# Optimization experiments

Measured on AMD Instinct MI355X. Metric: run time of the kernel, lower is better.

The kernel has to match this reference:

```python
import jax, jax.numpy as jnp
import numpy as np
from jax import lax

HEADS = 8
DIM_HEAD = 64
DIM = HEADS * DIM_HEAD  # 512


def _dwconv(x_nchw, w):
    # depthwise 3x3, stride 1, pad 1 (SAME), groups = channels
    return lax.conv_general_dilated(
        x_nchw, w, window_strides=(1, 1), padding='SAME',
        feature_group_count=x_nchw.shape[1],
        dimension_numbers=('NCHW', 'OIHW', 'NCHW'))


def setup_inputs() -> dict:
    key = jax.random.key(0)
    ks = jax.random.split(key, 9)
    b, h, w, c = 4, 256, 256, DIM
    s = 1.0 / np.sqrt(c)
    return {
        'x_in':    jax.random.normal(ks[0], (b, h, w, c), jnp.float32),
        'Wq':      jax.random.normal(ks[1], (c, DIM), jnp.float32) * s,
        'Wk':      jax.random.normal(ks[2], (c, DIM), jnp.float32) * s,
        'Wv':      jax.random.normal(ks[3], (c, DIM), jnp.float32) * s,
        'rescale': jnp.ones((HEADS, 1, 1), jnp.float32),
        'proj_w':  jax.random.normal(ks[4], (DIM, c), jnp.float32) * s,
        'proj_b':  jnp.zeros((c,), jnp.float32),
        'conv1_w': jax.random.normal(ks[5], (c, 1, 3, 3), jnp.float32) * (1.0 / 3.0),
        'conv2_w': jax.random.normal(ks[6], (c, 1, 3, 3), jnp.float32) * (1.0 / 3.0),
    }


def reference(x_in, Wq, Wk, Wv, rescale, proj_w, proj_b, conv1_w, conv2_w):
    b, h, w, c = x_in.shape
    n = h * w
    x = x_in.reshape(b, n, c)
    q_inp = x @ Wq  # [b, n, heads*d]
    k_inp = x @ Wk
    v_inp = x @ Wv

    def heads_dn(t):  # [b, n, heads*d] -> [b, heads, d, n]
        return t.reshape(b, n, HEADS, DIM_HEAD).transpose(0, 2, 3, 1)

    q = heads_dn(q_inp)
    k = heads_dn(k_inp)
    v = heads_dn(v_inp)

    # L2-normalize along token axis (F.normalize, eps=1e-12)
    qn = q / jnp.maximum(jnp.linalg.norm(q, axis=-1, keepdims=True), 1e-12)
    kn = k / jnp.maximum(jnp.linalg.norm(k, axis=-1, keepdims=True), 1e-12)

    # channel attention: [b, heads, d, d]
    attn = jnp.einsum('bhdn,bhen->bhde', kn, qn) * rescale
    attn = jax.nn.softmax(attn, axis=-1)
    xo = jnp.einsum('bhde,bhen->bhdn', attn, v)  # [b, heads, d, n]

    xo = xo.transpose(0, 3, 1, 2).reshape(b, n, HEADS * DIM_HEAD)
    out_c = (xo @ proj_w + proj_b).reshape(b, h, w, c)

    # depthwise conv positional embedding on v_inp
    vp = v_inp.reshape(b, h, w, c).transpose(0, 3, 1, 2)  # NCHW
    vp = _dwconv(vp, conv1_w)
    vp = jax.nn.gelu(vp, approximate=False)
    vp = _dwconv(vp, conv2_w)
    out_p = vp.transpose(0, 2, 3, 1)

    return out_c + out_p
```

## Files before the change

### kernel.cpp

```cpp
#include <hip/hip_runtime.h>
#include <math.h>

typedef unsigned short u16;
typedef unsigned int   u32;
typedef __attribute__((ext_vector_type(4))) float f32x4;
typedef __attribute__((ext_vector_type(8))) short bf16x8;
typedef __attribute__((ext_vector_type(8))) u16   u16x8;
typedef __attribute__((ext_vector_type(4))) u16   u16x4;

#define DEVI static __device__ __forceinline__

DEVI float bf2f(u16 a){ u32 u=((u32)a)<<16; float f; __builtin_memcpy(&f,&u,4); return f; }
DEVI u16 f2bf(float f){ u32 u; __builtin_memcpy(&u,&f,4); u=u+0x7fffu+((u>>16)&1u); return (u16)(u>>16); }

DEVI void gload16(const u16* src, u16* lds){
  __builtin_amdgcn_global_load_lds((const __attribute__((address_space(1))) u32*)src,
                                   (__attribute__((address_space(3))) u32*)lds, 16, 0, 0);
}

__global__ void k_wvt(const float* __restrict__ Wv, u16* __restrict__ WvT){
  int n = blockIdx.x;
  for (int k = threadIdx.x; k < 512; k += 256)
    WvT[(size_t)n*512 + k] = f2bf(Wv[(size_t)k*512 + n]);
}
__global__ void k_wrep(const float* __restrict__ w1, const float* __restrict__ w2, float* __restrict__ wt){
  int s = blockIdx.x/9, tap = blockIdx.x%9, c = threadIdx.x;
  const float* w = s ? w2 : w1;
  wt[(size_t)(s*9+tap)*512 + c] = w[(size_t)c*9 + tap];
}

__global__ __launch_bounds__(1024, 4) void k_gemm_v(const float* __restrict__ x, const u16* __restrict__ WvT,
                                                    u16* __restrict__ v, u16* __restrict__ xbT){
  __shared__ __align__(16) u16 Al[128*64];
  __shared__ __align__(16) u16 Bl[512*64];
  const int tid = threadIdx.x;
  const int l = tid & 63, w = tid >> 6;
  const int wr = w >> 3, wc = w & 7;
  const long r0 = (long)blockIdx.x * 128;
  f32x4 acc[4][4] = {};
  const int arow = tid >> 3, ac = tid & 7;
  const float* xp = x + (r0 + arow)*512 + ac*8;
  f32x4 va = *(const f32x4*)xp, vb = *(const f32x4*)(xp+4);
  for (int k0 = 0; k0 < 512; k0 += 64){
    {
      u16x8 o;
      o[0]=f2bf(va.x); o[1]=f2bf(va.y); o[2]=f2bf(va.z); o[3]=f2bf(va.w);
      o[4]=f2bf(vb.x); o[5]=f2bf(vb.y); o[6]=f2bf(vb.z); o[7]=f2bf(vb.w);
      *(u16x8*)&Al[arow*64 + ((ac ^ (arow&7))*8)] = o;
    }
    if (k0 < 448){
      va = *(const f32x4*)(xp + k0 + 64);
      vb = *(const f32x4*)(xp + k0 + 68);
    }
    #pragma unroll
    for (int i = 0; i < 4; ++i){
      int blkrow = w*32 + i*8;
      int r = blkrow + (l>>3);
      const u16* src = WvT + (size_t)r*512 + k0 + (((l&7) ^ ((l>>3)&7))*8);
      gload16(src, &Bl[blkrow*64]);
    }
    __syncthreads();
    #pragma unroll
    for (int ks = 0; ks < 2; ++ks){
      bf16x8 af[4], bfr[4];
      #pragma unroll
      for (int mf = 0; mf < 4; ++mf){
        int row = wr*64 + mf*16 + (l&15);
        af[mf] = *(const bf16x8*)&Al[row*64 + (((ks*4 + (l>>4)) ^ (row&7))*8)];
      }
      #pragma unroll
      for (int nf = 0; nf < 4; ++nf){
        int row = wc*64 + nf*16 + (l&15);
        bfr[nf] = *(const bf16x8*)&Bl[row*64 + (((ks*4 + (l>>4)) ^ (row&7))*8)];
      }
      #pragma unroll
      for (int mf = 0; mf < 4; ++mf)
        #pragma unroll
        for (int nf = 0; nf < 4; ++nf)
          acc[mf][nf] = __builtin_amdgcn_mfma_f32_16x16x32_bf16(af[mf], bfr[nf], acc[mf][nf], 0,0,0);
    }
    {
      int chloc = tid & 63, tg = tid >> 6;
      u16x8 o;
      #pragma unroll
      for (int j = 0; j < 8; ++j){
        int tok = tg*8 + j;
        o[j] = Al[tok*64 + (((chloc>>3) ^ (tok&7))*8) + (chloc&7)];
      }
      *(u16x8*)(xbT + (size_t)(k0 + chloc)*262144 + r0 + tg*8) = o;
    }
    __syncthreads();
  }
  #pragma unroll
  for (int mf = 0; mf < 4; ++mf)
    #pragma unroll
    for (int nf = 0; nf < 4; ++nf){
      int col = wc*64 + nf*16 + (l&15);
      #pragma unroll
      for (int j = 0; j < 4; ++j){
        long row = r0 + wr*64 + mf*16 + (l>>4)*4 + j;
        v[(size_t)row*512 + col] = f2bf(acc[mf][nf][j]);
      }
    }
}

__global__ __launch_bounds__(1024, 4) void k_syrk(const u16* __restrict__ xbT, float* __restrict__ P){
  __shared__ __align__(16) u16 AL[256*64];
  __shared__ __align__(16) u16 BL[256*64];
  const int bid = blockIdx.x;
  const int cs = bid & 63, combo = (bid>>6)%3, b = bid/192;
  const int hA = (combo==2) ? 1 : 0;
  const int tid = threadIdx.x;
  const int l = tid & 63, w = tid>>6, wi = w>>2, wj = w&3;
  const long tokb0 = (long)b*65536 + (long)cs*1024;
  const u16* Bread = (combo==1) ? BL : AL;
  f32x4 acc[4][4] = {};
  for (int st = 0; st < 16; ++st){
    const long tokb = tokb0 + st*64;
    #pragma unroll
    for (int i = 0; i < 2; ++i){
      int blkrow = w*16 + i*8;
      int r = blkrow + (l>>3);
      const u16* src = xbT + (size_t)(hA*256 + r)*262144 + tokb + (((l&7) ^ ((l>>3)&7))*8);
      gload16(src, &AL[blkrow*64]);
    }
    if (combo == 1){
      #pragma unroll
      for (int i = 0; i < 2; ++i){
        int blkrow = w*16 + i*8;
        int r = blkrow + (l>>3);
        const u16* src = xbT + (size_t)(256 + r)*262144 + tokb + (((l&7) ^ ((l>>3)&7))*8);
        gload16(src, &BL[blkrow*64]);
      }
    }
    __syncthreads();
    #pragma unroll
    for (int ks = 0; ks < 2; ++ks){
      bf16x8 af[4], bfr[4];
      #pragma unroll
      for (int mf = 0; mf < 4; ++mf){
        int row = wi*64 + mf*16 + (l&15);
        af[mf] = *(const bf16x8*)&AL[row*64 + (((ks*4 + (l>>4)) ^ (row&7))*8)];
      }
      #pragma unroll
      for (int nf = 0; nf < 4; ++nf){
        int row = wj*64 + nf*16 + (l&15);
        bfr[nf] = *(const bf16x8*)&Bread[row*64 + (((ks*4 + (l>>4)) ^ (row&7))*8)];
      }
      #pragma unroll
      for (int mf = 0; mf < 4; ++mf)
        #pragma unroll
        for (int nf = 0; nf < 4; ++nf)
          acc[mf][nf] = __builtin_amdgcn_mfma_f32_16x16x32_bf16(af[mf], bfr[nf], acc[mf][nf], 0,0,0);
    }
    __syncthreads();
  }
  float* Pb = P + (size_t)bid*65536;
  #pragma unroll
  for (int mf = 0; mf < 4; ++mf)
    #pragma unroll
    for (int nf = 0; nf < 4; ++nf)
      #pragma unroll
      for (int j = 0; j < 4; ++j){
        int il = wi*64 + mf*16 + (l>>4)*4 + j;
        int jl = wj*64 + nf*16 + (l&15);
        Pb[il*256 + jl] = acc[mf][nf][j];
      }
}

__global__ void k_sred(const float* __restrict__ P, float* __restrict__ S){
  int bid = blockIdx.x;
  int il = bid & 255, combo = (bid>>8)%3, b = bid/768;
  int hi = (combo==2)?1:0, hj = (combo==0)?0:1;
  int jl = threadIdx.x;
  float s = 0.f;
  for (int cs = 0; cs < 64; ++cs)
    s += P[((size_t)(b*192 + combo*64 + cs))*65536 + il*256 + jl];
  int I = hi*256 + il, J = hj*256 + jl;
  S[((size_t)b*512 + I)*512 + J] = s;
  if (combo == 1) S[((size_t)b*512 + J)*512 + I] = s;
}

__global__ __launch_bounds__(256) void k_a1(const float* __restrict__ S, const float* __restrict__ Wq,
                                            const float* __restrict__ Wk, float* __restrict__ T, float* __restrict__ U){
  int bid = blockIdx.x;
  int b = bid>>6, rem = bid&63, which = rem>>5, rbase = (rem&31)*16;
  const float* W = which ? Wk : Wq;
  float* O = which ? U : T;
  int tid = threadIdx.x;
  int rg = tid>>6, c0 = (tid&63)*8;
  const float* Sr = S + (size_t)b*262144 + (size_t)(rbase + rg*4)*512;
  float acc[4][8] = {};
  for (int k = 0; k < 512; ++k){
    float s0 = Sr[k], s1 = Sr[512+k], s2 = Sr[1024+k], s3 = Sr[1536+k];
    f32x4 wa = *(const f32x4*)(W + (size_t)k*512 + c0);
    f32x4 wb = *(const f32x4*)(W + (size_t)k*512 + c0 + 4);
    #pragma unroll
    for (int j = 0; j < 4; ++j){
      acc[0][j]   += s0*wa[j]; acc[1][j]   += s1*wa[j]; acc[2][j]   += s2*wa[j]; acc[3][j]   += s3*wa[j];
      acc[0][4+j] += s0*wb[j]; acc[1][4+j] += s1*wb[j]; acc[2][4+j] += s2*wb[j]; acc[3][4+j] += s3*wb[j];
    }
  }
  float* Ob = O + (size_t)b*262144;
  #pragma unroll
  for (int i = 0; i < 4; ++i){
    f32x4 o0, o1;
    o0.x=acc[i][0]; o0.y=acc[i][1]; o0.z=acc[i][2]; o0.w=acc[i][3];
    o1.x=acc[i][4]; o1.y=acc[i][5]; o1.z=acc[i][6]; o1.w=acc[i][7];
    *(f32x4*)(Ob + (size_t)(rbase+rg*4+i)*512 + c0)     = o0;
    *(f32x4*)(Ob + (size_t)(rbase+rg*4+i)*512 + c0 + 4) = o1;
  }
}

__global__ void k_a2(const float* __restrict__ Wq, const float* __restrict__ Wk,
                     const float* __restrict__ T, const float* __restrict__ U,
                     float* __restrict__ G, float* __restrict__ q2, float* __restrict__ k2){
  int b = blockIdx.x>>3, h = blockIdx.x&7;
  int tid = threadIdx.x;
  int d0 = (tid>>4)*4, e0 = (tid&15)*4;
  const float* Tb = T + (size_t)b*262144;
  float acc[4][4] = {};
  for (int i = 0; i < 512; ++i){
    f32x4 wk = *(const f32x4*)(Wk + (size_t)i*512 + h*64 + d0);
    f32x4 tv = *(const f32x4*)(Tb + (size_t)i*512 + h*64 + e0);
    #pragma unroll
    for (int di = 0; di < 4; ++di)
      #pragma unroll
      for (int ej = 0; ej < 4; ++ej) acc[di][ej] += wk[di]*tv[ej];
  }
  float* Gb = G + ((size_t)(b*8+h))*4096;
  #pragma unroll
  for (int di = 0; di < 4; ++di)
    #pragma unroll
    for (int ej = 0; ej < 4; ++ej) Gb[(d0+di)*64 + e0+ej] = acc[di][ej];
  if (tid < 64){
    int e = tid; float a = 0.f;
    for (int j = 0; j < 512; ++j) a += Wq[(size_t)j*512 + h*64 + e] * Tb[(size_t)j*512 + h*64 + e];
    q2[b*512 + h*64 + e] = a;
  } else if (tid < 128){
    int d = tid - 64; float a = 0.f;
    const float* Ub = U + (size_t)b*262144;
    for (int j = 0; j < 512; ++j) a += Wk[(size_t)j*512 + h*64 + d] * Ub[(size_t)j*512 + h*64 + d];
    k2[b*512 + h*64 + d] = a;
  }
}

__global__ void k_a3(const float* __restrict__ G, const float* __restrict__ resc,
                     const float* __restrict__ q2, const float* __restrict__ k2, float* __restrict__ Aa){
  int b = blockIdx.x>>3, h = blockIdx.x&7;
  int d = threadIdx.x;
  const float* g = G + ((size_t)(b*8+h))*4096 + d*64;
  float kn = fmaxf(sqrtf(k2[b*512 + h*64 + d]), 1e-12f);
  float sc = resc[h] / kn;
  float m = -3.4e38f;
  for (int e = 0; e < 64; ++e){
    float qn = fmaxf(sqrtf(q2[b*512 + h*64 + e]), 1e-12f);
    m = fmaxf(m, g[e]*sc/qn);
  }
  float ssum = 0.f;
  for (int e = 0; e < 64; ++e){
    float qn = fmaxf(sqrtf(q2[b*512 + h*64 + e]), 1e-12f);
    ssum += expf(g[e]*sc/qn - m);
  }
  float inv = 1.0f/ssum;
  float* ao = Aa + ((size_t)(b*8+h))*4096 + d*64;
  for (int e = 0; e < 64; ++e){
    float qn = fmaxf(sqrtf(q2[b*512 + h*64 + e]), 1e-12f);
    ao[e] = expf(g[e]*sc/qn - m)*inv;
  }
}

__global__ void k_a4(const float* __restrict__ Aa, const float* __restrict__ pw, u16* __restrict__ MT){
  int bid = blockIdx.x;
  int jt = bid&3, h = (bid>>2)&7, b = bid>>5;
  int tid = threadIdx.x;
  int j = jt*128 + (tid&127), eh = tid>>7;
  const float* Ab = Aa + ((size_t)(b*8+h))*4096;
  float acc[32] = {};
  for (int d = 0; d < 64; ++d){
    float p = pw[(size_t)(h*64+d)*512 + j];
    const float* ar = Ab + d*64 + eh*32;
    #pragma unroll
    for (int q = 0; q < 8; ++q){
      f32x4 pa = *(const f32x4*)(ar + q*4);
      acc[q*4+0] += pa.x*p; acc[q*4+1] += pa.y*p; acc[q*4+2] += pa.z*p; acc[q*4+3] += pa.w*p;
    }
  }
  u16* mo = MT + (size_t)b*262144 + (size_t)j*512 + h*64 + eh*32;
  #pragma unroll
  for (int q = 0; q < 16; ++q){
    u32 pk = (u32)f2bf(acc[2*q]) | ((u32)f2bf(acc[2*q+1])<<16);
    *(u32*)&mo[2*q] = pk;
  }
}

__global__ __launch_bounds__(256) void k_conv_fused(const u16* __restrict__ v, const float* __restrict__ wt,
                                                    u16* __restrict__ cbuf){
  __shared__ float vtf[400*16];
  __shared__ float t1f[324*16];
  const int logical = (blockIdx.x & 7)*4096 + (blockIdx.x >> 3);
  const int g = logical & 31, tx = (logical>>5)&15, ty = (logical>>9)&15, b = logical>>13;
  const int c0 = g*16, oy0 = ty*16, ox0 = tx*16;
  const int tid = threadIdx.x;
  const int quad = tid & 3;

  for (int k = 0; k < 7; ++k){
    int q = tid + k*256; if (q >= 1600) break;
    int pos = q >> 2;
    int ly = pos / 20, lx = pos - ly*20;
    int gy = oy0 - 2 + ly, gx = ox0 - 2 + lx;
    f32x4 val = {};
    if (gy >= 0 && gy < 256 && gx >= 0 && gx < 256){
      u16x4 raw = *(const u16x4*)(v + ((size_t)(b*65536 + gy*256 + gx))*512 + c0 + quad*4);
      val.x = bf2f(raw[0]); val.y = bf2f(raw[1]); val.z = bf2f(raw[2]); val.w = bf2f(raw[3]);
    }
    *(f32x4*)&vtf[pos*16 + quad*4] = val;
  }

  f32x4 wq[9];
  #pragma unroll
  for (int tap = 0; tap < 9; ++tap)
    wq[tap] = *(const f32x4*)(wt + (size_t)tap*512 + c0 + quad*4);
  __syncthreads();

  for (int k = 0; k < 6; ++k){
    int q = tid + k*256; if (q >= 1296) break;
    int pos = q >> 2;
    int y1 = pos / 18, x1 = pos - y1*18;
    int gy1 = oy0 - 1 + y1, gx1 = ox0 - 1 + x1;
    bool inimg = (gy1 >= 0 && gy1 < 256 && gx1 >= 0 && gx1 < 256);
    const float* base = &vtf[(y1*20 + x1)*16 + quad*4];
    float acc[4] = {};
    #pragma unroll
    for (int tap = 0; tap < 9; ++tap){
      int dy = tap/3, dx = tap - dy*3;
      f32x4 vv = *(const f32x4*)(base + (dy*20 + dx)*16);
      #pragma unroll
      for (int j = 0; j < 4; ++j) acc[j] += vv[j]*wq[tap][j];
    }
    f32x4 o;
    #pragma unroll
    for (int j = 0; j < 4; ++j){
      float a = acc[j];
      float gl = a / (1.0f + __expf(-1.5957691216f*a*(1.0f + 0.044715f*a*a)));
      o[j] = inimg ? gl : 0.0f;
    }
    *(f32x4*)&t1f[pos*16 + quad*4] = o;
  }

  #pragma unroll
  for (int tap = 0; tap < 9; ++tap)
    wq[tap] = *(const f32x4*)(wt + (size_t)(9+tap)*512 + c0 + quad*4);
  __syncthreads();

  #pragma unroll
  for (int k = 0; k < 4; ++k){
    int q = tid + k*256;
    int pos = q >> 2;
    int y2 = pos >> 4, x2 = pos & 15;
    const float* base = &t1f[(y2*18 + x2)*16 + quad*4];
    float acc[4] = {};
    #pragma unroll
    for (int tap = 0; tap < 9; ++tap){
      int dy = tap/3, dx = tap - dy*3;
      f32x4 tt = *(const f32x4*)(base + (dy*18 + dx)*16);
      #pragma unroll
      for (int j = 0; j < 4; ++j) acc[j] += tt[j]*wq[tap][j];
    }
    u16x4 o;
    #pragma unroll
    for (int j = 0; j < 4; ++j) o[j] = f2bf(acc[j]);
    size_t tok = (size_t)b*65536 + (size_t)(oy0+y2)*256 + (ox0+x2);
    *(u16x4*)(cbuf + tok*512 + c0 + quad*4) = o;
  }
}

__global__ __launch_bounds__(512, 2) void k_gemm_out(const u16* __restrict__ v, const u16* __restrict__ MT,
                                                     const float* __restrict__ proj_b, const u16* __restrict__ cbuf,
                                                     float* __restrict__ out){
  extern __shared__ __align__(16) u16 sm[];
  const int tid = threadIdx.x;
  const int l = tid & 63, w = tid >> 6;
  const int wr = w >> 2, wc = w & 3;
  const int bid = blockIdx.x;
  const int wg = (bid & 7)*256 + (bid >> 3);
  const long r0 = (long)(wg >> 1) * 256;
  const int  c0b = (wg & 1) * 256;
  const int  b = (int)(r0 >> 16);
  const u16* Mb = MT + (size_t)b*262144;
  f32x4 acc[8][4] = {};

  auto STAGE = [&](int buf, int k0){
    u16* Ab = sm + buf*16384;
    u16* Bb = sm + 32768 + buf*16384;
    #pragma unroll
    for (int i = 0; i < 4; ++i){
      int blkrow = w*32 + i*8;
      int r = blkrow + (l>>3);
      gload16(v + (size_t)(r0 + r)*512 + k0 + (((l&7) ^ (r&7))*8), Ab + blkrow*64);
    }
    #pragma unroll
    for (int i = 0; i < 4; ++i){
      int blkrow = w*32 + i*8;
      int r = blkrow + (l>>3);
      gload16(Mb + (size_t)(c0b + r)*512 + k0 + (((l&7) ^ (r&7))*8), Bb + blkrow*64);
    }
  };

  STAGE(0, 0);
  __syncthreads();
  for (int t = 0; t < 8; ++t){
    const int cur = t & 1;
    if (t < 7) STAGE(cur^1, (t+1)*64);
    const u16* Al = sm + cur*16384;
    const u16* Bl = sm + 32768 + cur*16384;
    #pragma unroll
    for (int ks = 0; ks < 2; ++ks){
      bf16x8 bfr[4];
      #pragma unroll
      for (int nf = 0; nf < 4; ++nf){
        int row = wc*64 + nf*16 + (l&15);
        bfr[nf] = *(const bf16x8*)&Bl[row*64 + (((ks*4 + (l>>4)) ^ (row&7))*8)];
      }
      #pragma unroll
      for (int mf = 0; mf < 8; ++mf){
        int row = wr*128 + mf*16 + (l&15);
        bf16x8 af = *(const bf16x8*)&Al[row*64 + (((ks*4 + (l>>4)) ^ (row&7))*8)];
        #pragma unroll
        for (int nf = 0; nf < 4; ++nf)
          acc[mf][nf] = __builtin_amdgcn_mfma_f32_16x16x32_bf16(af, bfr[nf], acc[mf][nf], 0,0,0);
      }
    }
    __syncthreads();
  }
  #pragma unroll
  for (int mf = 0; mf < 8; ++mf)
    #pragma unroll
    for (int nf = 0; nf < 4; ++nf){
      int col = c0b + wc*64 + nf*16 + (l&15);
      float pb = proj_b[col];
      #pragma unroll
      for (int j = 0; j < 4; ++j){
        long row = r0 + wr*128 + mf*16 + (l>>4)*4 + j;
        out[(size_t)row*512 + col] = acc[mf][nf][j] + pb + bf2f(cbuf[(size_t)row*512 + col]);
      }
    }
}

extern "C" void kernel_launch(void* const* d_in, const int* in_sizes, int n_in,
                              void* d_out, int out_size, void* d_ws, size_t ws_size,
                              hipStream_t stream){
  const float* x   = (const float*)d_in[0];
  const float* Wq  = (const float*)d_in[1];
  const float* Wk  = (const float*)d_in[2];
  const float* Wv  = (const float*)d_in[3];
  const float* rsc = (const float*)d_in[4];
  const float* pw  = (const float*)d_in[5];
  const float* pb  = (const float*)d_in[6];
  const float* w1  = (const float*)d_in[7];
  const float* w2  = (const float*)d_in[8];
  float* out = (float*)d_out;
  char* ws = (char*)d_ws;

  const size_t MB256 = 268435456;
  u16*   v    = (u16*)ws;
  u16*   xbT  = (u16*)(ws + MB256);
  u16*   cbuf = xbT;
  char*  sm0  = ws + 2*MB256;
  float* P    = (float*)d_out;

  float* S   = (float*)(sm0);
  float* Tm  = (float*)(sm0 + 4194304);
  float* Um  = (float*)(sm0 + 8388608);
  float* G   = (float*)(sm0 + 12582912);
  float* Aa  = (float*)(sm0 + 13107200);
  float* q2  = (float*)(sm0 + 13631488);
  float* k2  = (float*)(sm0 + 13639680);
  u16*   MT  = (u16*)  (sm0 + 13647872);
  u16*   WvT = (u16*)  (sm0 + 15745024);
  float* wt  = (float*)(sm0 + 16269312);

  k_wvt <<<512, 256, 0, stream>>>(Wv, WvT);
  k_wrep<<<18, 512, 0, stream>>>(w1, w2, wt);
  k_gemm_v<<<2048, 1024, 0, stream>>>(x, WvT, v, xbT);
  k_syrk<<<768, 1024, 0, stream>>>(xbT, P);
  k_sred<<<3072, 256, 0, stream>>>(P, S);
  k_a1<<<256, 256, 0, stream>>>(S, Wq, Wk, Tm, Um);
  k_a2<<<32, 256, 0, stream>>>(Wq, Wk, Tm, Um, G, q2, k2);
  k_a3<<<32, 64, 0, stream>>>(G, rsc, q2, k2, Aa);
  k_a4<<<128, 256, 0, stream>>>(Aa, pw, MT);
  k_conv_fused<<<32768, 256, 0, stream>>>(v, wt, cbuf);
  k_gemm_out<<<2048, 512, 131072, stream>>>(v, MT, pb, cbuf, out);
}
```

Baseline: 1.536 ms.

## Split fused depthwise conv into two sliding-window register kernels

Replaces the single LDS-tiled fused conv+GELU+conv kernel with two separate kernels. Each thread walks 64 pixels along a row for 4 channels and keeps a 3x3 register window, so shared memory, barriers and halo recomputation go away. The intermediate GELU output is stored as bf16 in the output buffer and read back by the second kernel. This adds a full extra write and read of a 256MB intermediate, and each thread issues strided 8-byte loads across three rows.

```diff
diff --git a/kernel.cpp b/kernel.cpp
--- a/kernel.cpp
+++ b/kernel.cpp
@@ -294,84 +294,108 @@
   }
 }
 
-__global__ __launch_bounds__(256) void k_conv_fused(const u16* __restrict__ v, const float* __restrict__ wt,
-                                                    u16* __restrict__ cbuf){
-  __shared__ float vtf[400*16];
-  __shared__ float t1f[324*16];
-  const int logical = (blockIdx.x & 7)*4096 + (blockIdx.x >> 3);
-  const int g = logical & 31, tx = (logical>>5)&15, ty = (logical>>9)&15, b = logical>>13;
-  const int c0 = g*16, oy0 = ty*16, ox0 = tx*16;
+__global__ __launch_bounds__(256) void k_conv1(const u16* __restrict__ v, const float* __restrict__ wt,
+                                               u16* __restrict__ t){
+  const int logical = (blockIdx.x & 7)*256 + (blockIdx.x >> 3);
+  const int xs = logical & 3, yp = (logical>>2) & 127, b = logical >> 9;
   const int tid = threadIdx.x;
-  const int quad = tid & 3;
-
-  for (int k = 0; k < 7; ++k){
-    int q = tid + k*256; if (q >= 1600) break;
-    int pos = q >> 2;
-    int ly = pos / 20, lx = pos - ly*20;
-    int gy = oy0 - 2 + ly, gx = ox0 - 2 + lx;
-    f32x4 val = {};
-    if (gy >= 0 && gy < 256 && gx >= 0 && gx < 256){
-      u16x4 raw = *(const u16x4*)(v + ((size_t)(b*65536 + gy*256 + gx))*512 + c0 + quad*4);
-      val.x = bf2f(raw[0]); val.y = bf2f(raw[1]); val.z = bf2f(raw[2]); val.w = bf2f(raw[3]);
-    }
-    *(f32x4*)&vtf[pos*16 + quad*4] = val;
-  }
-
+  const int ch4 = (tid & 127)*4;
+  const int yy = yp*2 + (tid>>7);
+  const int x0 = xs*64;
+  const u16* vb = v + ((size_t)b*65536)*512 + ch4;
   f32x4 wq[9];
   #pragma unroll
-  for (int tap = 0; tap < 9; ++tap)
-    wq[tap] = *(const f32x4*)(wt + (size_t)tap*512 + c0 + quad*4);
-  __syncthreads();
-
-  for (int k = 0; k < 6; ++k){
-    int q = tid + k*256; if (q >= 1296) break;
-    int pos = q >> 2;
-    int y1 = pos / 18, x1 = pos - y1*18;
-    int gy1 = oy0 - 1 + y1, gx1 = ox0 - 1 + x1;
-    bool inimg = (gy1 >= 0 && gy1 < 256 && gx1 >= 0 && gx1 < 256);
-    const float* base = &vtf[(y1*20 + x1)*16 + quad*4];
-    float acc[4] = {};
-    #pragma unroll
-    for (int tap = 0; tap < 9; ++tap){
-      int dy = tap/3, dx = tap - dy*3;
-      f32x4 vv = *(const f32x4*)(base + (dy*20 + dx)*16);
-      #pragma unroll
-      for (int j = 0; j < 4; ++j) acc[j] += vv[j]*wq[tap][j];
-    }
-    f32x4 o;
+  for (int tap = 0; tap < 9; ++tap) wq[tap] = *(const f32x4*)(wt + (size_t)tap*512 + ch4);
+  const bool rok[3] = { yy > 0, true, yy < 255 };
+
+  f32x4 win[3][3];
+  #pragma unroll
+  for (int r = 0; r < 3; ++r)
+    #pragma unroll
+    for (int c = 0; c < 2; ++c){
+      f32x4 z = {};
+      int xx = x0 - 1 + c;
+      if (rok[r] && xx >= 0){
+        u16x4 raw = *(const u16x4*)(vb + ((size_t)((yy-1+r)*256 + xx))*512);
+        z.x=bf2f(raw[0]); z.y=bf2f(raw[1]); z.z=bf2f(raw[2]); z.w=bf2f(raw[3]);
+      }
+      win[r][c] = z;
+    }
+  for (int xi = 0; xi < 64; ++xi){
+    int x = x0 + xi;
+    #pragma unroll
+    for (int r = 0; r < 3; ++r){
+      f32x4 z = {};
+      if (rok[r] && x+1 < 256){
+        u16x4 raw = *(const u16x4*)(vb + ((size_t)((yy-1+r)*256 + x+1))*512);
+        z.x=bf2f(raw[0]); z.y=bf2f(raw[1]); z.z=bf2f(raw[2]); z.w=bf2f(raw[3]);
+      }
+      win[r][2] = z;
+    }
+    u16x4 o;
     #pragma unroll
     for (int j = 0; j < 4; ++j){
-      float a = acc[j];
+      float a = win[0][0][j]*wq[0][j] + win[0][1][j]*wq[1][j] + win[0][2][j]*wq[2][j]
+              + win[1][0][j]*wq[3][j] + win[1][1][j]*wq[4][j] + win[1][2][j]*wq[5][j]
+              + win[2][0][j]*wq[6][j] + win[2][1][j]*wq[7][j] + win[2][2][j]*wq[8][j];
       float gl = a / (1.0f + __expf(-1.5957691216f*a*(1.0f + 0.044715f*a*a)));
-      o[j] = inimg ? gl : 0.0f;
-    }
-    *(f32x4*)&t1f[pos*16 + quad*4] = o;
-  }
-
-  #pragma unroll
-  for (int tap = 0; tap < 9; ++tap)
-    wq[tap] = *(const f32x4*)(wt + (size_t)(9+tap)*512 + c0 + quad*4);
-  __syncthreads();
-
-  #pragma unroll
-  for (int k = 0; k < 4; ++k){
-    int q = tid + k*256;
-    int pos = q >> 2;
-    int y2 = pos >> 4, x2 = pos & 15;
-    const float* base = &t1f[(y2*18 + x2)*16 + quad*4];
-    float acc[4] = {};
-    #pragma unroll
-    for (int tap = 0; tap < 9; ++tap){
-      int dy = tap/3, dx = tap - dy*3;
-      f32x4 tt = *(const f32x4*)(base + (dy*18 + dx)*16);
-      #pragma unroll
-      for (int j = 0; j < 4; ++j) acc[j] += tt[j]*wq[tap][j];
+      o[j] = f2bf(gl);
+    }
+    *(u16x4*)(t + ((size_t)b*65536 + yy*256 + x)*512 + ch4) = o;
+    #pragma unroll
+    for (int r = 0; r < 3; ++r){ win[r][0] = win[r][1]; win[r][1] = win[r][2]; }
+  }
+}
+
+__global__ __launch_bounds__(256) void k_conv2(const u16* __restrict__ t, const float* __restrict__ wt,
+                                               u16* __restrict__ cbuf){
+  const int logical = (blockIdx.x & 7)*256 + (blockIdx.x >> 3);
+  const int xs = logical & 3, yp = (logical>>2) & 127, b = logical >> 9;
+  const int tid = threadIdx.x;
+  const int ch4 = (tid & 127)*4;
+  const int yy = yp*2 + (tid>>7);
+  const int x0 = xs*64;
+  const u16* tb = t + ((size_t)b*65536)*512 + ch4;
+  f32x4 wq[9];
+  #pragma unroll
+  for (int tap = 0; tap < 9; ++tap) wq[tap] = *(const f32x4*)(wt + (size_t)(9+tap)*512 + ch4);
+  const bool rok[3] = { yy > 0, true, yy < 255 };
+
+  f32x4 win[3][3];
+  #pragma unroll
+  for (int r = 0; r < 3; ++r)
+    #pragma unroll
+    for (int c = 0; c < 2; ++c){
+      f32x4 z = {};
+      int xx = x0 - 1 + c;
+      if (rok[r] && xx >= 0){
+        u16x4 raw = *(const u16x4*)(tb + ((size_t)((yy-1+r)*256 + xx))*512);
+        z.x=bf2f(raw[0]); z.y=bf2f(raw[1]); z.z=bf2f(raw[2]); z.w=bf2f(raw[3]);
+      }
+      win[r][c] = z;
+    }
+  for (int xi = 0; xi < 64; ++xi){
+    int x = x0 + xi;
+    #pragma unroll
+    for (int r = 0; r < 3; ++r){
+      f32x4 z = {};
+      if (rok[r] && x+1 < 256){
+        u16x4 raw = *(const u16x4*)(tb + ((size_t)((yy-1+r)*256 + x+1))*512);
+        z.x=bf2f(raw[0]); z.y=bf2f(raw[1]); z.z=bf2f(raw[2]); z.w=bf2f(raw[3]);
+      }
+      win[r][2] = z;
     }
     u16x4 o;
     #pragma unroll
-    for (int j = 0; j < 4; ++j) o[j] = f2bf(acc[j]);
-    size_t tok = (size_t)b*65536 + (size_t)(oy0+y2)*256 + (ox0+x2);
-    *(u16x4*)(cbuf + tok*512 + c0 + quad*4) = o;
+    for (int j = 0; j < 4; ++j){
+      float a = win[0][0][j]*wq[0][j] + win[0][1][j]*wq[1][j] + win[0][2][j]*wq[2][j]
+              + win[1][0][j]*wq[3][j] + win[1][1][j]*wq[4][j] + win[1][2][j]*wq[5][j]
+              + win[2][0][j]*wq[6][j] + win[2][1][j]*wq[7][j] + win[2][2][j]*wq[8][j];
+      o[j] = f2bf(a);
+    }
+    *(u16x4*)(cbuf + ((size_t)b*65536 + yy*256 + x)*512 + ch4) = o;
+    #pragma unroll
+    for (int r = 0; r < 3; ++r){ win[r][0] = win[r][1]; win[r][1] = win[r][2]; }
   }
 }
 
@@ -468,6 +492,7 @@
   u16*   cbuf = xbT;
   char*  sm0  = ws + 2*MB256;
   float* P    = (float*)d_out;
+  u16*   t    = (u16*)d_out;
 
   float* S   = (float*)(sm0);
   float* Tm  = (float*)(sm0 + 4194304);
@@ -489,6 +514,7 @@
   k_a2<<<32, 256, 0, stream>>>(Wq, Wk, Tm, Um, G, q2, k2);
   k_a3<<<32, 64, 0, stream>>>(G, rsc, q2, k2, Aa);
   k_a4<<<128, 256, 0, stream>>>(Aa, pw, MT);
-  k_conv_fused<<<32768, 256, 0, stream>>>(v, wt, cbuf);
+  k_conv1<<<2048, 256, 0, stream>>>(v, wt, t);
+  k_conv2<<<2048, 256, 0, stream>>>(t, wt, cbuf);
   k_gemm_out<<<2048, 512, 131072, stream>>>(v, MT, pb, cbuf, out);
 }
```

Result: slower. 1.692 ms (+10.2%).

## Double-buffer LDS in V-projection GEMM with 512-thread blocks and K=32 steps

Applied to the files above, without the earlier changes.

Rewrites the x@Wv GEMM kernel to use double-buffered dynamic shared memory with a K-step of 32. The global loads for the next step are issued before the MFMA work on the current one, so one barrier per step replaces two. Block size drops from 1024 to 512 threads, and each wave now computes 128x64 with 8x4 accumulators instead of 64x64. This is meant to overlap memory traffic with compute and improve register reuse of the B fragments. In exchange it uses 80KB of LDS, which limits blocks per CU, and twice as many loop iterations.

```diff
diff --git a/kernel.cpp b/kernel.cpp
--- a/kernel.cpp
+++ b/kernel.cpp
@@ -29,76 +29,80 @@
   wt[(size_t)(s*9+tap)*512 + c] = w[(size_t)c*9 + tap];
 }
 
-__global__ __launch_bounds__(1024, 4) void k_gemm_v(const float* __restrict__ x, const u16* __restrict__ WvT,
-                                                    u16* __restrict__ v, u16* __restrict__ xbT){
-  __shared__ __align__(16) u16 Al[128*64];
-  __shared__ __align__(16) u16 Bl[512*64];
+__global__ __launch_bounds__(512) void k_gemm_v(const float* __restrict__ x, const u16* __restrict__ WvT,
+                                                u16* __restrict__ v, u16* __restrict__ xbT){
+  extern __shared__ __align__(16) u16 sm[];
   const int tid = threadIdx.x;
   const int l = tid & 63, w = tid >> 6;
-  const int wr = w >> 3, wc = w & 7;
   const long r0 = (long)blockIdx.x * 128;
-  f32x4 acc[4][4] = {};
-  const int arow = tid >> 3, ac = tid & 7;
+  f32x4 acc[8][4] = {};
+
+  const int arow = tid >> 2, ac = tid & 3;
   const float* xp = x + (r0 + arow)*512 + ac*8;
-  f32x4 va = *(const f32x4*)xp, vb = *(const f32x4*)(xp+4);
-  for (int k0 = 0; k0 < 512; k0 += 64){
+  f32x4 rAa, rAb;
+
+  auto LOADA = [&](int kk){ rAa = *(const f32x4*)(xp + kk); rAb = *(const f32x4*)(xp + kk + 4); };
+  auto WRITEA = [&](int buf){
+    u16x8 o;
+    o[0]=f2bf(rAa.x); o[1]=f2bf(rAa.y); o[2]=f2bf(rAa.z); o[3]=f2bf(rAa.w);
+    o[4]=f2bf(rAb.x); o[5]=f2bf(rAb.y); o[6]=f2bf(rAb.z); o[7]=f2bf(rAb.w);
+    *(u16x8*)&sm[buf*4096 + arow*32 + ((ac ^ ((arow>>1)&3))*8)] = o;
+  };
+  auto GLOADB = [&](int buf, int kk){
+    #pragma unroll
+    for (int i = 0; i < 4; ++i){
+      int blkrow = w*64 + i*16;
+      int r = blkrow + (l>>2);
+      const u16* src = WvT + (size_t)r*512 + kk + (((l&3) ^ ((l>>3)&3))*8);
+      gload16(src, &sm[8192 + buf*16384 + blkrow*32]);
+    }
+  };
+
+  LOADA(0); WRITEA(0); LOADA(32); GLOADB(0, 0);
+  __syncthreads();
+  for (int t = 0; t < 16; ++t){
+    const int cur = t & 1;
+    if (t < 15){
+      WRITEA(cur^1);
+      if (t < 14) LOADA((t+2)*32);
+      GLOADB(cur^1, (t+1)*32);
+    }
+    const u16* Al = sm + cur*4096;
+    const u16* Bl = sm + 8192 + cur*16384;
+    bf16x8 bfr[4];
+    #pragma unroll
+    for (int nf = 0; nf < 4; ++nf){
+      int row = w*64 + nf*16 + (l&15);
+      bfr[nf] = *(const bf16x8*)&Bl[row*32 + (((l>>4) ^ ((row>>1)&3))*8)];
+    }
+    #pragma unroll
+    for (int mf = 0; mf < 8; ++mf){
+      int row = mf*16 + (l&15);
+      bf16x8 af = *(const bf16x8*)&Al[row*32 + (((l>>4) ^ ((row>>1)&3))*8)];
+      #pragma unroll
+      for (int nf = 0; nf < 4; ++nf)
+        acc[mf][nf] = __builtin_amdgcn_mfma_f32_16x16x32_bf16(af, bfr[nf], acc[mf][nf], 0,0,0);
+    }
     {
-      u16x8 o;
-      o[0]=f2bf(va.x); o[1]=f2bf(va.y); o[2]=f2bf(va.z); o[3]=f2bf(va.w);
-      o[4]=f2bf(vb.x); o[5]=f2bf(vb.y); o[6]=f2bf(vb.z); o[7]=f2bf(vb.w);
-      *(u16x8*)&Al[arow*64 + ((ac ^ (arow&7))*8)] = o;
-    }
-    if (k0 < 448){
-      va = *(const f32x4*)(xp + k0 + 64);
-      vb = *(const f32x4*)(xp + k0 + 68);
-    }
-    #pragma unroll
-    for (int i = 0; i < 4; ++i){
-      int blkrow = w*32 + i*8;
-      int r = blkrow + (l>>3);
-      const u16* src = WvT + (size_t)r*512 + k0 + (((l&7) ^ ((l>>3)&7))*8);
-      gload16(src, &Bl[blkrow*64]);
-    }
-    __syncthreads();
-    #pragma unroll
-    for (int ks = 0; ks < 2; ++ks){
-      bf16x8 af[4], bfr[4];
-      #pragma unroll
-      for (int mf = 0; mf < 4; ++mf){
-        int row = wr*64 + mf*16 + (l&15);
-        af[mf] = *(const bf16x8*)&Al[row*64 + (((ks*4 + (l>>4)) ^ (row&7))*8)];
-      }
-      #pragma unroll
-      for (int nf = 0; nf < 4; ++nf){
-        int row = wc*64 + nf*16 + (l&15);
-        bfr[nf] = *(const bf16x8*)&Bl[row*64 + (((ks*4 + (l>>4)) ^ (row&7))*8)];
-      }
-      #pragma unroll
-      for (int mf = 0; mf < 4; ++mf)
-        #pragma unroll
-        for (int nf = 0; nf < 4; ++nf)
-          acc[mf][nf] = __builtin_amdgcn_mfma_f32_16x16x32_bf16(af[mf], bfr[nf], acc[mf][nf], 0,0,0);
-    }
-    {
-      int chloc = tid & 63, tg = tid >> 6;
+      int chloc = tid & 31, tg = tid >> 5;
       u16x8 o;
       #pragma unroll
       for (int j = 0; j < 8; ++j){
         int tok = tg*8 + j;
-        o[j] = Al[tok*64 + (((chloc>>3) ^ (tok&7))*8) + (chloc&7)];
-      }
-      *(u16x8*)(xbT + (size_t)(k0 + chloc)*262144 + r0 + tg*8) = o;
+        o[j] = Al[tok*32 + (((chloc>>3) ^ ((tok>>1)&3))*8) + (chloc&7)];
+      }
+      *(u16x8*)(xbT + (size_t)(t*32 + chloc)*262144 + r0 + tg*8) = o;
     }
     __syncthreads();
   }
   #pragma unroll
-  for (int mf = 0; mf < 4; ++mf)
+  for (int mf = 0; mf < 8; ++mf)
     #pragma unroll
     for (int nf = 0; nf < 4; ++nf){
-      int col = wc*64 + nf*16 + (l&15);
+      int col = w*64 + nf*16 + (l&15);
       #pragma unroll
       for (int j = 0; j < 4; ++j){
-        long row = r0 + wr*64 + mf*16 + (l>>4)*4 + j;
+        long row = r0 + mf*16 + (l>>4)*4 + j;
         v[(size_t)row*512 + col] = f2bf(acc[mf][nf][j]);
       }
     }
@@ -482,7 +486,7 @@
 
   k_wvt <<<512, 256, 0, stream>>>(Wv, WvT);
   k_wrep<<<18, 512, 0, stream>>>(w1, w2, wt);
-  k_gemm_v<<<2048, 1024, 0, stream>>>(x, WvT, v, xbT);
+  k_gemm_v<<<2048, 512, 81920, stream>>>(x, WvT, v, xbT);
   k_syrk<<<768, 1024, 0, stream>>>(xbT, P);
   k_sred<<<3072, 256, 0, stream>>>(P, S);
   k_a1<<<256, 256, 0, stream>>>(S, Wq, Wk, Tm, Um);
```

New measurement: 1.513 ms. About the same (-1.5%).
